# Kernel optimization log

Hardware: AMD Instinct MI355X
Metric: run time of the kernel (lower is better)

## Reference

```python
import jax, jax.numpy as jnp
import numpy as np

EPS = 1e-6     # vnn EPS
BN_EPS = 1e-5  # torch BatchNorm eps


def _vn_batchnorm(x, gamma, beta):
    # x: (B, C, 3, ...). BatchNorm on vector norms (training-mode batch stats).
    norm = jnp.linalg.norm(x, axis=2) + EPS                # (B, C, ...)
    axes = (0,) + tuple(range(2, norm.ndim))
    mean = norm.mean(axis=axes, keepdims=True)
    var = norm.var(axis=axes, keepdims=True)               # biased var, as torch training BN
    shape = (1, -1) + (1,) * (norm.ndim - 2)
    norm_bn = (norm - mean) / jnp.sqrt(var + BN_EPS) * gamma.reshape(shape) + beta.reshape(shape)
    return x / jnp.expand_dims(norm, 2) * jnp.expand_dims(norm_bn, 2)


def _vn_linear_leaky(x, Wf, Wd, gamma, beta):
    # VNLinearLeakyReLU with negative_slope = 0.0
    p = jnp.einsum('oc,bc...->bo...', Wf, x)
    p = _vn_batchnorm(p, gamma, beta)
    d = jnp.einsum('oc,bc...->bo...', Wd, x)
    dot = jnp.sum(p * d, axis=2, keepdims=True)
    dsq = jnp.sum(d * d, axis=2, keepdims=True)
    mask = (dot >= 0).astype(x.dtype)
    return mask * p + (1.0 - mask) * (p - (dot / (dsq + EPS)) * d)


def _graph_feature_cross(x, k):
    # x: (B, 3, N) -> (B, 3, 3, N, k)  channels = [nbr - x, x, x cross nbr]
    xt = jnp.swapaxes(x, 1, 2)                             # (B, N, 3)
    inner = -2.0 * jnp.einsum('bnc,bmc->bnm', xt, xt)      # (B, N, N)
    xx = jnp.sum(x * x, axis=1)                            # (B, N)
    pd = -xx[:, :, None] - inner - xx[:, None, :]          # negative squared distance
    idx = jax.lax.top_k(pd, k)[1]                          # (B, N, k)
    nbr = jax.vmap(lambda pts, i: pts[i])(xt, idx)         # (B, N, k, 3)
    nbr = nbr[:, :, :, None, :]                            # (B, N, k, 1, 3)
    ctr = jnp.broadcast_to(xt[:, :, None, None, :], nbr.shape)
    cross = jnp.cross(nbr, ctr)
    feat = jnp.concatenate([nbr - ctr, ctr, cross], axis=3)  # (B, N, k, 3, 3)
    return jnp.transpose(feat, (0, 3, 4, 1, 2))            # (B, 3, 3, N, k)


def _forward(point_cloud, Wf0, Wd0, g0, b0, Wf1, Wd1, g1, b1, gbn1, bbn1, Wf2, Wd2, g2, b2):
    x = jnp.swapaxes(point_cloud, 1, 2)                    # (B, 3, N)
    num_points = x.shape[1]                                # = 3, faithful to source
    k = min(5, num_points - 1)                             # = 2
    feat = _graph_feature_cross(x, k)                      # (B, 3, 3, N, k)
    out = _vn_linear_leaky(feat, Wf0, Wd0, g0, b0)         # (B, 21, 3, N, k)
    out = out.mean(axis=-1)                                # mean_pool over k -> (B, 21, 3, N)
    out = _vn_linear_leaky(out, Wf1, Wd1, g1, b1)
    out = _vn_batchnorm(out, gbn1, bbn1)
    out = _vn_linear_leaky(out, Wf2, Wd2, g2, b2)          # (B, 4, 3, N)
    # dropout: eval-mode identity
    return out.mean(axis=-1)[:, :3]                        # (B, 3, 3)


def setup_inputs() -> dict:
    key = jax.random.key(0)
    ks = jax.random.split(key, 8)
    B, N = 16, 4096
    C = 21  # 64 // 3
    Co = 4  # 12 // 3
    f32 = jnp.float32
    s3 = 1.0 / np.sqrt(3.0)
    sC = 1.0 / np.sqrt(C)
    return {
        'point_cloud': jax.random.normal(ks[0], (B, N, 3), f32),
        'Wf0': jax.random.normal(ks[1], (C, 3), f32) * s3,
        'Wd0': jax.random.normal(ks[2], (C, 3), f32) * s3,
        'g0': jnp.ones((C,), f32), 'b0': jnp.zeros((C,), f32),
        'Wf1': jax.random.normal(ks[3], (C, C), f32) * sC,
        'Wd1': jax.random.normal(ks[4], (C, C), f32) * sC,
        'g1': jnp.ones((C,), f32), 'b1': jnp.zeros((C,), f32),
        'gbn1': jnp.ones((C,), f32), 'bbn1': jnp.zeros((C,), f32),
        'Wf2': jax.random.normal(ks[5], (Co, C), f32) * sC,
        'Wd2': jax.random.normal(ks[6], (Co, C), f32) * sC,
        'g2': jnp.ones((Co,), f32), 'b2': jnp.zeros((Co,), f32),
    }


def reference(point_cloud, Wf0, Wd0, g0, b0, Wf1, Wd1, g1, b1, gbn1, bbn1, Wf2, Wd2, g2, b2):
    return _forward(point_cloud, Wf0, Wd0, g0, b0, Wf1, Wd1, g1, b1, gbn1, bbn1, Wf2, Wd2, g2, b2)
```

## Files before the change

### kernel.cpp

```cpp
#include <hip/hip_runtime.h>
#include <math.h>

#define B 16
#define N 4096
#define NPTS (B * N)
#define NBK 2048
#define NBT 1024
#define EPSF 1e-6f
#define S8(i) ((i) * 8)

__device__ __forceinline__ float waveReduceSum(float v) {
#pragma unroll
    for (int m = 32; m > 0; m >>= 1) v += __shfl_xor(v, m, 64);
    return v;
}

__device__ __forceinline__ void leaky3(float px, float py, float pz,
                                       float dx, float dy, float dz, float s,
                                       float& ox, float& oy, float& oz) {
    float dotr = px * dx + py * dy + pz * dz;
    float dsq = dx * dx + dy * dy + dz * dz;
    float dot = s * dotr;
    float coef = (dot >= 0.f) ? 0.f : (dot / (dsq + EPSF));
    ox = s * px - coef * dx;
    oy = s * py - coef * dy;
    oz = s * pz - coef * dz;
}

__device__ __forceinline__ void mk_muisd_b(const double* st, int cnt, double M,
                                           float* smu, float* sisd) {
    const int i = threadIdx.x;
    if (i < cnt) {
        double s1 = 0.0, s2 = 0.0;
#pragma unroll
        for (int b = 0; b < B; ++b) {
            s1 += st[S8(b * 2 * cnt + i)];
            s2 += st[S8(b * 2 * cnt + cnt + i)];
        }
        double m = s1 / M;
        double v = s2 / M - m * m;
        smu[i] = (float)m;
        sisd[i] = (float)(1.0 / sqrt(v + 1e-5));
    }
}

struct Feat {
    float cx, cy, cz, e0x, e0y, e0z, e2x, e2y, e2z;
};

__device__ __forceinline__ Feat make_feat(const float* __restrict__ pc,
                                          const int* __restrict__ nbr, int pid) {
    const int b = pid >> 12, n = pid & (N - 1);
    const float* base = pc + (size_t)b * (3 * N);
    Feat f;
    f.cx = base[3 * n];
    f.cy = base[3 * n + 1];
    f.cz = base[3 * n + 2];
    const int jn = nbr[pid];
    float nx = base[3 * jn], ny = base[3 * jn + 1], nz = base[3 * jn + 2];
    f.e0x = nx - f.cx;
    f.e0y = ny - f.cy;
    f.e0z = nz - f.cz;
    f.e2x = ny * f.cz - nz * f.cy;
    f.e2y = nz * f.cx - nx * f.cz;
    f.e2z = nx * f.cy - ny * f.cx;
    return f;
}

#define QW 8
__global__ __launch_bounds__(256) void k_knn(const float* __restrict__ pc,
                                             const float* __restrict__ Wf0,
                                             int* __restrict__ nbrbest,
                                             double* __restrict__ st0) {
    __shared__ float sx[N], sy[N], sz[N];
    __shared__ float ws0[63], sred[168];
    const int b = blockIdx.x >> 7;
    const int qblk = (blockIdx.x & 127) * 32;
    const float* base = pc + (size_t)b * (N * 3);
    for (int j = threadIdx.x; j < N; j += 256) {
        sx[j] = base[3 * j + 0];
        sy[j] = base[3 * j + 1];
        sz[j] = base[3 * j + 2];
    }
    if (threadIdx.x < 63) ws0[threadIdx.x] = Wf0[threadIdx.x];
    __syncthreads();
    const int wid = threadIdx.x >> 6, lane = threadIdx.x & 63;
    const int q0 = qblk + wid * QW;
    float qx[QW], qy[QW], qz[QW], bv[QW];
    int bi[QW], bq[QW];
#pragma unroll
    for (int q = 0; q < QW; ++q) {
        qx[q] = sx[q0 + q];
        qy[q] = sy[q0 + q];
        qz[q] = sz[q0 + q];
        bv[q] = -3.0e38f;
        bi[q] = 0;
    }
#pragma unroll 4
    for (int ch = 0; ch < N / 64; ++ch) {
        const int j = ch * 64 + lane;
        const float xd = sx[j], yd = sy[j], zd = sz[j];
        const float nr2h = -0.5f * (xd * xd + yd * yd + zd * zd);
#pragma unroll
        for (int q = 0; q < QW; ++q) {
            float pd = fmaf(qx[q], xd, fmaf(qy[q], yd, fmaf(qz[q], zd, nr2h)));
            bool upd = (pd > bv[q]) && (j != q0 + q);
            bv[q] = upd ? pd : bv[q];
            bi[q] = upd ? j : bi[q];
        }
    }
#pragma unroll
    for (int q = 0; q < QW; ++q) {
        float a0v = bv[q], a1v = -3.0e38f;
        int a0i = bi[q], a1i = 0x7fffffff;
#pragma unroll
        for (int m = 1; m < 64; m <<= 1) {
            float b0v = __shfl_xor(a0v, m, 64), b1v = __shfl_xor(a1v, m, 64);
            int b0i = __shfl_xor(a0i, m, 64), b1i = __shfl_xor(a1i, m, 64);
            bool bf = (b0v > a0v) || (b0v == a0v && b0i < a0i);
            float c0v = bf ? a0v : b0v;
            int c0i = bf ? a0i : b0i;
            float c1v = bf ? b1v : a1v;
            int c1i = bf ? b1i : a1i;
            a0v = bf ? b0v : a0v;
            a0i = bf ? b0i : a0i;
            bool cf = (c0v > c1v) || (c0v == c1v && c0i < c1i);
            a1v = cf ? c0v : c1v;
            a1i = cf ? c0i : c1i;
        }
        const int i0 = a0i, i1 = a1i;
        double dxa = (double)qx[q] - (double)sx[i0];
        double dya = (double)qy[q] - (double)sy[i0];
        double dza = (double)qz[q] - (double)sz[i0];
        double d0 = dxa * dxa + dya * dya + dza * dza;
        double dxb = (double)qx[q] - (double)sx[i1];
        double dyb = (double)qy[q] - (double)sy[i1];
        double dzb = (double)qz[q] - (double)sz[i1];
        double d1 = dxb * dxb + dyb * dyb + dzb * dzb;
        bool take1 = (d1 < d0) || (d1 == d0 && i1 < i0);
        int best = take1 ? i1 : i0;
        bq[q] = best;
        if (lane == 0) nbrbest[(size_t)b * N + q0 + q] = best;
    }
    if (lane < 21) {
        float s1 = 0.f, s2 = 0.f;
        const float w0 = ws0[3 * lane], w1 = ws0[3 * lane + 1], w2 = ws0[3 * lane + 2];
#pragma unroll
        for (int q = 0; q < QW; ++q) {
            const int sq = q0 + q, jn = bq[q];
            const float cx = sx[sq], cy = sy[sq], cz = sz[sq];
            const float nx = sx[jn], ny = sy[jn], nz = sz[jn];
            const float e0x = nx - cx, e0y = ny - cy, e0z = nz - cz;
            const float e2x = ny * cz - nz * cy;
            const float e2y = nz * cx - nx * cz;
            const float e2z = nx * cy - ny * cx;
            float pSx = w1 * cx, pSy = w1 * cy, pSz = w1 * cz;
            float nS = sqrtf(pSx * pSx + pSy * pSy + pSz * pSz) + EPSF;
            float px = w0 * e0x + w1 * cx + w2 * e2x;
            float py = w0 * e0y + w1 * cy + w2 * e2y;
            float pz = w0 * e0z + w1 * cz + w2 * e2z;
            float nN = sqrtf(px * px + py * py + pz * pz) + EPSF;
            s1 += nS + nN;
            s2 += nS * nS + nN * nN;
        }
        sred[wid * 42 + lane] = s1;
        sred[wid * 42 + 21 + lane] = s2;
    }
    __syncthreads();
    if (threadIdx.x < 42) {
        float p = sred[threadIdx.x] + sred[42 + threadIdx.x] +
                  sred[84 + threadIdx.x] + sred[126 + threadIdx.x];
        atomicAdd(&st0[S8(b * 42 + threadIdx.x)], (double)p);
    }
}

__global__ __launch_bounds__(256) void k_l0st1(
    const float* __restrict__ pc, const int* __restrict__ nbr,
    const float* __restrict__ Wf0, const float* __restrict__ Wd0,
    const float* __restrict__ g0, const float* __restrict__ b0,
    const float* __restrict__ Wf1, const double* __restrict__ st0,
    float* __restrict__ xbuf, double* __restrict__ st1) {
    __shared__ float wf0[63], wd0[63], wf1[441], gg[21], bbs[21], mu[21], isd[21];
    __shared__ float xs[63 * 64];
    if (threadIdx.x < 63) {
        wf0[threadIdx.x] = Wf0[threadIdx.x];
        wd0[threadIdx.x] = Wd0[threadIdx.x];
    }
    for (int i = threadIdx.x; i < 441; i += 256) wf1[i] = Wf1[i];
    if (threadIdx.x < 21) {
        gg[threadIdx.x] = g0[threadIdx.x];
        bbs[threadIdx.x] = b0[threadIdx.x];
    }
    mk_muisd_b(st0, 21, (double)NPTS * 2.0, mu, isd);
    __syncthreads();
    const int lane = threadIdx.x & 63, grp = threadIdx.x >> 6;
    const int pid = blockIdx.x * 64 + lane;
    const int bb = blockIdx.x >> 6;
    Feat f = make_feat(pc, nbr, pid);
    const int cbase = grp * 6;
#pragma unroll
    for (int k = 0; k < 6; ++k) {
        const int c = cbase + k;
        if (c >= 21) break;
        float w0 = wf0[3 * c], w1 = wf0[3 * c + 1], w2 = wf0[3 * c + 2];
        float u0 = wd0[3 * c], u1 = wd0[3 * c + 1], u2 = wd0[3 * c + 2];
        float pSx = w1 * f.cx, pSy = w1 * f.cy, pSz = w1 * f.cz;
        float nS = sqrtf(pSx * pSx + pSy * pSy + pSz * pSz) + EPSF;
        float sS = ((nS - mu[c]) * isd[c] * gg[c] + bbs[c]) / nS;
        float oSx, oSy, oSz;
        leaky3(pSx, pSy, pSz, u1 * f.cx, u1 * f.cy, u1 * f.cz, sS, oSx, oSy, oSz);
        float px = w0 * f.e0x + w1 * f.cx + w2 * f.e2x;
        float py = w0 * f.e0y + w1 * f.cy + w2 * f.e2y;
        float pz = w0 * f.e0z + w1 * f.cz + w2 * f.e2z;
        float dx = u0 * f.e0x + u1 * f.cx + u2 * f.e2x;
        float dy = u0 * f.e0y + u1 * f.cy + u2 * f.e2y;
        float dz = u0 * f.e0z + u1 * f.cz + u2 * f.e2z;
        float nN = sqrtf(px * px + py * py + pz * pz) + EPSF;
        float sN = ((nN - mu[c]) * isd[c] * gg[c] + bbs[c]) / nN;
        float oNx, oNy, oNz;
        leaky3(px, py, pz, dx, dy, dz, sN, oNx, oNy, oNz);
        float x0 = 0.5f * (oSx + oNx), x1 = 0.5f * (oSy + oNy), x2 = 0.5f * (oSz + oNz);
        xs[(3 * c + 0) * 64 + lane] = x0;
        xs[(3 * c + 1) * 64 + lane] = x1;
        xs[(3 * c + 2) * 64 + lane] = x2;
        xbuf[(size_t)(3 * c + 0) * NPTS + pid] = x0;
        xbuf[(size_t)(3 * c + 1) * NPTS + pid] = x1;
        xbuf[(size_t)(3 * c + 2) * NPTS + pid] = x2;
    }
    __syncthreads();
    float xl[63];
#pragma unroll
    for (int ff = 0; ff < 63; ++ff) xl[ff] = xs[ff * 64 + lane];
#pragma unroll
    for (int k = 0; k < 6; ++k) {
        const int c = cbase + k;
        if (c >= 21) break;
        float p0 = 0.f, p1 = 0.f, p2 = 0.f;
#pragma unroll
        for (int j = 0; j < 21; ++j) {
            float w = wf1[c * 21 + j];
            p0 = fmaf(w, xl[3 * j + 0], p0);
            p1 = fmaf(w, xl[3 * j + 1], p1);
            p2 = fmaf(w, xl[3 * j + 2], p2);
        }
        float nn = sqrtf(p0 * p0 + p1 * p1 + p2 * p2) + EPSF;
        float r1 = waveReduceSum(nn);
        float r2 = waveReduceSum(nn * nn);
        if (lane == 0) {
            atomicAdd(&st1[S8(bb * 42 + c)], (double)r1);
            atomicAdd(&st1[S8(bb * 42 + 21 + c)], (double)r2);
        }
    }
}

__global__ __launch_bounds__(256) void k_l1stB(
    float* __restrict__ xbuf, const float* __restrict__ Wf1,
    const float* __restrict__ Wd1, const float* __restrict__ g1,
    const float* __restrict__ b1, const double* __restrict__ st1,
    double* __restrict__ stB) {
    __shared__ float wf1[441], wd1[441], gg[21], bbs[21], mu[21], isd[21];
    for (int i = threadIdx.x; i < 441; i += 256) {
        wf1[i] = Wf1[i];
        wd1[i] = Wd1[i];
    }
    if (threadIdx.x < 21) {
        gg[threadIdx.x] = g1[threadIdx.x];
        bbs[threadIdx.x] = b1[threadIdx.x];
    }
    mk_muisd_b(st1, 21, (double)NPTS, mu, isd);
    __syncthreads();
    const int lane = threadIdx.x & 63, grp = threadIdx.x >> 6;
    const int pid = blockIdx.x * 64 + lane;
    const int bb = blockIdx.x >> 6;
    float xl[63];
#pragma unroll
    for (int ff = 0; ff < 63; ++ff) xl[ff] = xbuf[(size_t)ff * NPTS + pid];
    __syncthreads();
    const int cbase = grp * 6;
#pragma unroll
    for (int k = 0; k < 6; ++k) {
        const int c = cbase + k;
        if (c >= 21) break;
        float p0 = 0.f, p1 = 0.f, p2 = 0.f, d0 = 0.f, d1 = 0.f, d2 = 0.f;
#pragma unroll
        for (int j = 0; j < 21; ++j) {
            float w = wf1[c * 21 + j], u = wd1[c * 21 + j];
            p0 = fmaf(w, xl[3 * j + 0], p0);
            p1 = fmaf(w, xl[3 * j + 1], p1);
            p2 = fmaf(w, xl[3 * j + 2], p2);
            d0 = fmaf(u, xl[3 * j + 0], d0);
            d1 = fmaf(u, xl[3 * j + 1], d1);
            d2 = fmaf(u, xl[3 * j + 2], d2);
        }
        float nn = sqrtf(p0 * p0 + p1 * p1 + p2 * p2) + EPSF;
        float s = ((nn - mu[c]) * isd[c] * gg[c] + bbs[c]) / nn;
        float ox, oy, oz;
        leaky3(p0, p1, p2, d0, d1, d2, s, ox, oy, oz);
        xbuf[(size_t)(3 * c + 0) * NPTS + pid] = ox;
        xbuf[(size_t)(3 * c + 1) * NPTS + pid] = oy;
        xbuf[(size_t)(3 * c + 2) * NPTS + pid] = oz;
        float on = sqrtf(ox * ox + oy * oy + oz * oz) + EPSF;
        float r1 = waveReduceSum(on);
        float r2 = waveReduceSum(on * on);
        if (lane == 0) {
            atomicAdd(&stB[S8(bb * 42 + c)], (double)r1);
            atomicAdd(&stB[S8(bb * 42 + 21 + c)], (double)r2);
        }
    }
}

__global__ __launch_bounds__(256) void k_bn1st2(
    const float* __restrict__ xbuf, const float* __restrict__ gbn,
    const float* __restrict__ bbn, const float* __restrict__ Wf2,
    const double* __restrict__ stB, double* __restrict__ st2) {
    __shared__ float wf2[63], gg[21], bbs[21], mu[21], isd[21];
    __shared__ float zs[63 * 64];
    if (threadIdx.x < 63) wf2[threadIdx.x] = Wf2[threadIdx.x];
    if (threadIdx.x < 21) {
        gg[threadIdx.x] = gbn[threadIdx.x];
        bbs[threadIdx.x] = bbn[threadIdx.x];
    }
    mk_muisd_b(stB, 21, (double)NPTS, mu, isd);
    __syncthreads();
    const int lane = threadIdx.x & 63, grp = threadIdx.x >> 6;
    const int pid = blockIdx.x * 64 + lane;
    const int bb = blockIdx.x >> 6;
    const int cbase = grp * 6;
#pragma unroll
    for (int k = 0; k < 6; ++k) {
        const int c = cbase + k;
        if (c >= 21) break;
        float y0 = xbuf[(size_t)(3 * c + 0) * NPTS + pid];
        float y1 = xbuf[(size_t)(3 * c + 1) * NPTS + pid];
        float y2 = xbuf[(size_t)(3 * c + 2) * NPTS + pid];
        float nn = sqrtf(y0 * y0 + y1 * y1 + y2 * y2) + EPSF;
        float sc = ((nn - mu[c]) * isd[c] * gg[c] + bbs[c]) / nn;
        zs[(3 * c + 0) * 64 + lane] = sc * y0;
        zs[(3 * c + 1) * 64 + lane] = sc * y1;
        zs[(3 * c + 2) * 64 + lane] = sc * y2;
    }
    __syncthreads();
    if (grp < 3) {
        float p0 = 0.f, p1 = 0.f, p2 = 0.f;
#pragma unroll
        for (int j = 0; j < 21; ++j) {
            float w = wf2[grp * 21 + j];
            p0 = fmaf(w, zs[(3 * j + 0) * 64 + lane], p0);
            p1 = fmaf(w, zs[(3 * j + 1) * 64 + lane], p1);
            p2 = fmaf(w, zs[(3 * j + 2) * 64 + lane], p2);
        }
        float nn = sqrtf(p0 * p0 + p1 * p1 + p2 * p2) + EPSF;
        float r1 = waveReduceSum(nn);
        float r2 = waveReduceSum(nn * nn);
        if (lane == 0) {
            atomicAdd(&st2[S8(bb * 6 + grp)], (double)r1);
            atomicAdd(&st2[S8(bb * 6 + 3 + grp)], (double)r2);
        }
    }
}

__global__ __launch_bounds__(256) void k_acc(
    const float* __restrict__ xbuf, const float* __restrict__ gbn,
    const float* __restrict__ bbn, const float* __restrict__ Wf2,
    const float* __restrict__ Wd2, const float* __restrict__ g2,
    const float* __restrict__ b2, const double* __restrict__ stB,
    const double* __restrict__ st2, double* __restrict__ acc) {
    __shared__ float wf2[63], wd2[63], gg[3], bbs[3];
    __shared__ float muB[21], isdB[21], gB[21], bB[21], mu2[3], isd2[3];
    if (threadIdx.x < 63) {
        wf2[threadIdx.x] = Wf2[threadIdx.x];
        wd2[threadIdx.x] = Wd2[threadIdx.x];
    }
    if (threadIdx.x < 21) {
        gB[threadIdx.x] = gbn[threadIdx.x];
        bB[threadIdx.x] = bbn[threadIdx.x];
    }
    if (threadIdx.x < 3) {
        gg[threadIdx.x] = g2[threadIdx.x];
        bbs[threadIdx.x] = b2[threadIdx.x];
    }
    mk_muisd_b(stB, 21, (double)NPTS, muB, isdB);
    mk_muisd_b(st2, 3, (double)NPTS, mu2, isd2);
    __syncthreads();
    const int lane = threadIdx.x & 63, grp = threadIdx.x >> 6;
    if (grp >= 3) return;
    const int pid = blockIdx.x * 64 + lane;
    const int bb = pid >> 12;
    float p0 = 0.f, p1 = 0.f, p2 = 0.f, d0 = 0.f, d1 = 0.f, d2 = 0.f;
#pragma unroll
    for (int j = 0; j < 21; ++j) {
        float y0 = xbuf[(size_t)(3 * j + 0) * NPTS + pid];
        float y1 = xbuf[(size_t)(3 * j + 1) * NPTS + pid];
        float y2 = xbuf[(size_t)(3 * j + 2) * NPTS + pid];
        float nn = sqrtf(y0 * y0 + y1 * y1 + y2 * y2) + EPSF;
        float sc = ((nn - muB[j]) * isdB[j] * gB[j] + bB[j]) / nn;
        float z0 = sc * y0, z1 = sc * y1, z2 = sc * y2;
        float w = wf2[grp * 21 + j], u = wd2[grp * 21 + j];
        p0 = fmaf(w, z0, p0);
        p1 = fmaf(w, z1, p1);
        p2 = fmaf(w, z2, p2);
        d0 = fmaf(u, z0, d0);
        d1 = fmaf(u, z1, d1);
        d2 = fmaf(u, z2, d2);
    }
    float nn = sqrtf(p0 * p0 + p1 * p1 + p2 * p2) + EPSF;
    float s = ((nn - mu2[grp]) * isd2[grp] * gg[grp] + bbs[grp]) / nn;
    float ox, oy, oz;
    leaky3(p0, p1, p2, d0, d1, d2, s, ox, oy, oz);
    float rx = waveReduceSum(ox);
    float ry = waveReduceSum(oy);
    float rz = waveReduceSum(oz);
    if (lane == 0) {
        atomicAdd(&acc[S8(bb * 9 + grp * 3 + 0)], (double)rx);
        atomicAdd(&acc[S8(bb * 9 + grp * 3 + 1)], (double)ry);
        atomicAdd(&acc[S8(bb * 9 + grp * 3 + 2)], (double)rz);
    }
}

__global__ void k_fin(const double* __restrict__ acc, float* __restrict__ out) {
    if (threadIdx.x < B * 9)
        out[threadIdx.x] = (float)(acc[S8(threadIdx.x)] * (1.0 / (double)N));
}

extern "C" void kernel_launch(void* const* d_in, const int* in_sizes, int n_in,
                              void* d_out, int out_size, void* d_ws, size_t ws_size,
                              hipStream_t stream) {
    const float* pc = (const float*)d_in[0];
    const float* Wf0 = (const float*)d_in[1];
    const float* Wd0 = (const float*)d_in[2];
    const float* g0 = (const float*)d_in[3];
    const float* b0 = (const float*)d_in[4];
    const float* Wf1 = (const float*)d_in[5];
    const float* Wd1 = (const float*)d_in[6];
    const float* g1 = (const float*)d_in[7];
    const float* b1 = (const float*)d_in[8];
    const float* gbn1 = (const float*)d_in[9];
    const float* bbn1 = (const float*)d_in[10];
    const float* Wf2 = (const float*)d_in[11];
    const float* Wd2 = (const float*)d_in[12];
    const float* g2 = (const float*)d_in[13];
    const float* b2 = (const float*)d_in[14];
    float* out = (float*)d_out;

    char* ws = (char*)d_ws;
    double* gws = (double*)ws;
    double* st0 = gws;
    double* st1 = gws + S8(672);
    double* stB = gws + S8(1344);
    double* st2 = gws + S8(2016);
    double* acc = gws + S8(2112);
    int* nbrbest = (int*)(ws + 262144);
    float* xbuf = (float*)(ws + 524288);

    hipMemsetAsync(d_ws, 0, 144384, stream);

    k_knn<<<NBK, 256, 0, stream>>>(pc, Wf0, nbrbest, st0);
    k_l0st1<<<NBT, 256, 0, stream>>>(pc, nbrbest, Wf0, Wd0, g0, b0, Wf1, st0,
                                     xbuf, st1);
    k_l1stB<<<NBT, 256, 0, stream>>>(xbuf, Wf1, Wd1, g1, b1, st1, stB);
    k_bn1st2<<<NBT, 256, 0, stream>>>(xbuf, gbn1, bbn1, Wf2, stB, st2);
    k_acc<<<NBT, 256, 0, stream>>>(xbuf, gbn1, bbn1, Wf2, Wd2, g2, b2, stB, st2, acc);
    k_fin<<<1, 256, 0, stream>>>(acc, out);
}
```

Before: 222.7 us.

## Fuse post-kNN layers into one cooperative kernel with grid syncs

Replaces the four per-layer kernels and the final reduction kernel with a single cooperative megakernel. It uses grid.sync at each batch-norm statistics barrier and keeps the per-point 63-float feature tile in shared memory across all stages. This removes the xbuf global round-trips and several kernel launches. In exchange it depends on all 1024 blocks being co-resident, and it falls back to the old kernels if the cooperative launch fails.

```diff
diff --git a/kernel.cpp b/kernel.cpp
--- a/kernel.cpp
+++ b/kernel.cpp
@@ -1,5 +1,8 @@
 #include <hip/hip_runtime.h>
+#include <hip/hip_cooperative_groups.h>
 #include <math.h>
+
+namespace cg = cooperative_groups;
 
 #define B 16
 #define N 4096
@@ -36,6 +39,24 @@
         for (int b = 0; b < B; ++b) {
             s1 += st[S8(b * 2 * cnt + i)];
             s2 += st[S8(b * 2 * cnt + cnt + i)];
+        }
+        double m = s1 / M;
+        double v = s2 / M - m * m;
+        smu[i] = (float)m;
+        sisd[i] = (float)(1.0 / sqrt(v + 1e-5));
+    }
+}
+
+__device__ __forceinline__ void mk_muisd_v(const double* st, int cnt, double M,
+                                           float* smu, float* sisd) {
+    const int i = threadIdx.x;
+    if (i < cnt) {
+        const volatile double* vst = (const volatile double*)st;
+        double s1 = 0.0, s2 = 0.0;
+#pragma unroll
+        for (int b = 0; b < B; ++b) {
+            s1 += vst[S8(b * 2 * cnt + i)];
+            s2 += vst[S8(b * 2 * cnt + cnt + i)];
         }
         double m = s1 / M;
         double v = s2 / M - m * m;
@@ -67,6 +88,30 @@
     return f;
 }
 
+__device__ __forceinline__ void l0_channel(const Feat& f, float w0, float w1,
+                                           float w2, float u0, float u1, float u2,
+                                           float mu, float isd, float g, float bb,
+                                           float& x0, float& x1, float& x2) {
+    float pSx = w1 * f.cx, pSy = w1 * f.cy, pSz = w1 * f.cz;
+    float nS = sqrtf(pSx * pSx + pSy * pSy + pSz * pSz) + EPSF;
+    float sS = ((nS - mu) * isd * g + bb) / nS;
+    float oSx, oSy, oSz;
+    leaky3(pSx, pSy, pSz, u1 * f.cx, u1 * f.cy, u1 * f.cz, sS, oSx, oSy, oSz);
+    float px = w0 * f.e0x + w1 * f.cx + w2 * f.e2x;
+    float py = w0 * f.e0y + w1 * f.cy + w2 * f.e2y;
+    float pz = w0 * f.e0z + w1 * f.cz + w2 * f.e2z;
+    float dx = u0 * f.e0x + u1 * f.cx + u2 * f.e2x;
+    float dy = u0 * f.e0y + u1 * f.cy + u2 * f.e2y;
+    float dz = u0 * f.e0z + u1 * f.cz + u2 * f.e2z;
+    float nN = sqrtf(px * px + py * py + pz * pz) + EPSF;
+    float sN = ((nN - mu) * isd * g + bb) / nN;
+    float oNx, oNy, oNz;
+    leaky3(px, py, pz, dx, dy, dz, sN, oNx, oNy, oNz);
+    x0 = 0.5f * (oSx + oNx);
+    x1 = 0.5f * (oSy + oNy);
+    x2 = 0.5f * (oSz + oNz);
+}
+
 #define QW 8
 __global__ __launch_bounds__(256) void k_knn(const float* __restrict__ pc,
                                              const float* __restrict__ Wf0,
@@ -174,6 +219,230 @@
     }
 }
 
+__global__ __launch_bounds__(256, 4) void k_mega(
+    const float* __restrict__ pc, const int* __restrict__ nbr,
+    const float* __restrict__ Wf0, const float* __restrict__ Wd0,
+    const float* __restrict__ g0, const float* __restrict__ b0,
+    const float* __restrict__ Wf1, const float* __restrict__ Wd1,
+    const float* __restrict__ g1, const float* __restrict__ b1,
+    const float* __restrict__ gbn1, const float* __restrict__ bbn1,
+    const float* __restrict__ Wf2, const float* __restrict__ Wd2,
+    const float* __restrict__ g2, const float* __restrict__ b2,
+    const double* __restrict__ st0, double* __restrict__ st1,
+    double* __restrict__ stB, double* __restrict__ st2,
+    double* __restrict__ acc, float* __restrict__ out) {
+    __shared__ float xs[63 * 64];
+    __shared__ float wf0[63], wd0[63], wf1[441], wd1[441], wf2[63], wd2[63];
+    __shared__ float g0s[21], b0s[21], g1s[21], b1s[21], gBs[21], bBs[21], g2s[3], b2s[3];
+    __shared__ float mu0[21], isd0[21], mu1[21], isd1[21], muB[21], isdB[21], mu2[3], isd2[3];
+    cg::grid_group grid = cg::this_grid();
+    const int lane = threadIdx.x & 63, grp = threadIdx.x >> 6;
+    const int pid = blockIdx.x * 64 + lane;
+    const int bb = blockIdx.x >> 6;
+    const int cbase = grp * 6;
+
+    if (threadIdx.x < 63) {
+        wf0[threadIdx.x] = Wf0[threadIdx.x];
+        wd0[threadIdx.x] = Wd0[threadIdx.x];
+        wf2[threadIdx.x] = Wf2[threadIdx.x];
+        wd2[threadIdx.x] = Wd2[threadIdx.x];
+    }
+    for (int i = threadIdx.x; i < 441; i += 256) {
+        wf1[i] = Wf1[i];
+        wd1[i] = Wd1[i];
+    }
+    if (threadIdx.x < 21) {
+        g0s[threadIdx.x] = g0[threadIdx.x];
+        b0s[threadIdx.x] = b0[threadIdx.x];
+        g1s[threadIdx.x] = g1[threadIdx.x];
+        b1s[threadIdx.x] = b1[threadIdx.x];
+        gBs[threadIdx.x] = gbn1[threadIdx.x];
+        bBs[threadIdx.x] = bbn1[threadIdx.x];
+    }
+    if (threadIdx.x < 3) {
+        g2s[threadIdx.x] = g2[threadIdx.x];
+        b2s[threadIdx.x] = b2[threadIdx.x];
+    }
+    mk_muisd_b(st0, 21, (double)NPTS * 2.0, mu0, isd0);
+    __syncthreads();
+
+    {
+        Feat f = make_feat(pc, nbr, pid);
+#pragma unroll
+        for (int k = 0; k < 6; ++k) {
+            const int c = cbase + k;
+            if (c >= 21) break;
+            float x0, x1, x2;
+            l0_channel(f, wf0[3 * c], wf0[3 * c + 1], wf0[3 * c + 2],
+                       wd0[3 * c], wd0[3 * c + 1], wd0[3 * c + 2],
+                       mu0[c], isd0[c], g0s[c], b0s[c], x0, x1, x2);
+            xs[(3 * c + 0) * 64 + lane] = x0;
+            xs[(3 * c + 1) * 64 + lane] = x1;
+            xs[(3 * c + 2) * 64 + lane] = x2;
+        }
+    }
+    __syncthreads();
+    {
+        float a0[6], a1[6], a2[6];
+#pragma unroll
+        for (int k = 0; k < 6; ++k) { a0[k] = 0.f; a1[k] = 0.f; a2[k] = 0.f; }
+        for (int j = 0; j < 21; ++j) {
+            float x0 = xs[(3 * j + 0) * 64 + lane];
+            float x1 = xs[(3 * j + 1) * 64 + lane];
+            float x2 = xs[(3 * j + 2) * 64 + lane];
+#pragma unroll
+            for (int k = 0; k < 6; ++k) {
+                int cc = cbase + k;
+                cc = cc < 21 ? cc : 20;
+                float w = wf1[cc * 21 + j];
+                a0[k] = fmaf(w, x0, a0[k]);
+                a1[k] = fmaf(w, x1, a1[k]);
+                a2[k] = fmaf(w, x2, a2[k]);
+            }
+        }
+#pragma unroll
+        for (int k = 0; k < 6; ++k) {
+            const int c = cbase + k;
+            if (c >= 21) break;
+            float nn = sqrtf(a0[k] * a0[k] + a1[k] * a1[k] + a2[k] * a2[k]) + EPSF;
+            float r1 = waveReduceSum(nn);
+            float r2 = waveReduceSum(nn * nn);
+            if (lane == 0) {
+                atomicAdd(&st1[S8(bb * 42 + c)], (double)r1);
+                atomicAdd(&st1[S8(bb * 42 + 21 + c)], (double)r2);
+            }
+        }
+    }
+    grid.sync();
+
+    mk_muisd_v(st1, 21, (double)NPTS, mu1, isd1);
+    __syncthreads();
+    {
+        float p0[6], p1[6], p2[6], q0[6], q1[6], q2[6];
+#pragma unroll
+        for (int k = 0; k < 6; ++k) {
+            p0[k] = 0.f; p1[k] = 0.f; p2[k] = 0.f;
+            q0[k] = 0.f; q1[k] = 0.f; q2[k] = 0.f;
+        }
+        for (int j = 0; j < 21; ++j) {
+            float x0 = xs[(3 * j + 0) * 64 + lane];
+            float x1 = xs[(3 * j + 1) * 64 + lane];
+            float x2 = xs[(3 * j + 2) * 64 + lane];
+#pragma unroll
+            for (int k = 0; k < 6; ++k) {
+                int cc = cbase + k;
+                cc = cc < 21 ? cc : 20;
+                float w = wf1[cc * 21 + j], u = wd1[cc * 21 + j];
+                p0[k] = fmaf(w, x0, p0[k]);
+                p1[k] = fmaf(w, x1, p1[k]);
+                p2[k] = fmaf(w, x2, p2[k]);
+                q0[k] = fmaf(u, x0, q0[k]);
+                q1[k] = fmaf(u, x1, q1[k]);
+                q2[k] = fmaf(u, x2, q2[k]);
+            }
+        }
+        float sn1[6], sn2[6];
+#pragma unroll
+        for (int k = 0; k < 6; ++k) {
+            int cc = cbase + k;
+            cc = cc < 21 ? cc : 20;
+            float nn = sqrtf(p0[k] * p0[k] + p1[k] * p1[k] + p2[k] * p2[k]) + EPSF;
+            float s = ((nn - mu1[cc]) * isd1[cc] * g1s[cc] + b1s[cc]) / nn;
+            float ox, oy, oz;
+            leaky3(p0[k], p1[k], p2[k], q0[k], q1[k], q2[k], s, ox, oy, oz);
+            p0[k] = ox; p1[k] = oy; p2[k] = oz;
+            float on = sqrtf(ox * ox + oy * oy + oz * oz) + EPSF;
+            sn1[k] = on;
+            sn2[k] = on * on;
+        }
+        __syncthreads();
+#pragma unroll
+        for (int k = 0; k < 6; ++k) {
+            const int c = cbase + k;
+            if (c >= 21) break;
+            xs[(3 * c + 0) * 64 + lane] = p0[k];
+            xs[(3 * c + 1) * 64 + lane] = p1[k];
+            xs[(3 * c + 2) * 64 + lane] = p2[k];
+            float r1 = waveReduceSum(sn1[k]);
+            float r2 = waveReduceSum(sn2[k]);
+            if (lane == 0) {
+                atomicAdd(&stB[S8(bb * 42 + c)], (double)r1);
+                atomicAdd(&stB[S8(bb * 42 + 21 + c)], (double)r2);
+            }
+        }
+    }
+    grid.sync();
+
+    mk_muisd_v(stB, 21, (double)NPTS, muB, isdB);
+    __syncthreads();
+#pragma unroll
+    for (int k = 0; k < 6; ++k) {
+        const int c = cbase + k;
+        if (c >= 21) break;
+        float y0 = xs[(3 * c + 0) * 64 + lane];
+        float y1 = xs[(3 * c + 1) * 64 + lane];
+        float y2 = xs[(3 * c + 2) * 64 + lane];
+        float nn = sqrtf(y0 * y0 + y1 * y1 + y2 * y2) + EPSF;
+        float sc = ((nn - muB[c]) * isdB[c] * gBs[c] + bBs[c]) / nn;
+        xs[(3 * c + 0) * 64 + lane] = sc * y0;
+        xs[(3 * c + 1) * 64 + lane] = sc * y1;
+        xs[(3 * c + 2) * 64 + lane] = sc * y2;
+    }
+    __syncthreads();
+    if (grp < 3) {
+        float p0 = 0.f, p1 = 0.f, p2 = 0.f;
+        for (int j = 0; j < 21; ++j) {
+            float w = wf2[grp * 21 + j];
+            p0 = fmaf(w, xs[(3 * j + 0) * 64 + lane], p0);
+            p1 = fmaf(w, xs[(3 * j + 1) * 64 + lane], p1);
+            p2 = fmaf(w, xs[(3 * j + 2) * 64 + lane], p2);
+        }
+        float nn = sqrtf(p0 * p0 + p1 * p1 + p2 * p2) + EPSF;
+        float r1 = waveReduceSum(nn);
+        float r2 = waveReduceSum(nn * nn);
+        if (lane == 0) {
+            atomicAdd(&st2[S8(bb * 6 + grp)], (double)r1);
+            atomicAdd(&st2[S8(bb * 6 + 3 + grp)], (double)r2);
+        }
+    }
+    grid.sync();
+
+    mk_muisd_v(st2, 3, (double)NPTS, mu2, isd2);
+    __syncthreads();
+    if (grp < 3) {
+        float p0 = 0.f, p1 = 0.f, p2 = 0.f, d0 = 0.f, d1 = 0.f, d2 = 0.f;
+        for (int j = 0; j < 21; ++j) {
+            float z0 = xs[(3 * j + 0) * 64 + lane];
+            float z1 = xs[(3 * j + 1) * 64 + lane];
+            float z2 = xs[(3 * j + 2) * 64 + lane];
+            float w = wf2[grp * 21 + j], u = wd2[grp * 21 + j];
+            p0 = fmaf(w, z0, p0);
+            p1 = fmaf(w, z1, p1);
+            p2 = fmaf(w, z2, p2);
+            d0 = fmaf(u, z0, d0);
+            d1 = fmaf(u, z1, d1);
+            d2 = fmaf(u, z2, d2);
+        }
+        float nn = sqrtf(p0 * p0 + p1 * p1 + p2 * p2) + EPSF;
+        float s = ((nn - mu2[grp]) * isd2[grp] * g2s[grp] + b2s[grp]) / nn;
+        float ox, oy, oz;
+        leaky3(p0, p1, p2, d0, d1, d2, s, ox, oy, oz);
+        float rx = waveReduceSum(ox);
+        float ry = waveReduceSum(oy);
+        float rz = waveReduceSum(oz);
+        if (lane == 0) {
+            atomicAdd(&acc[S8(bb * 9 + grp * 3 + 0)], (double)rx);
+            atomicAdd(&acc[S8(bb * 9 + grp * 3 + 1)], (double)ry);
+            atomicAdd(&acc[S8(bb * 9 + grp * 3 + 2)], (double)rz);
+        }
+    }
+    grid.sync();
+    if (blockIdx.x == 0 && threadIdx.x < B * 9) {
+        const volatile double* va = (const volatile double*)acc;
+        out[threadIdx.x] = (float)(va[S8(threadIdx.x)] * (1.0 / (double)N));
+    }
+}
+
 __global__ __launch_bounds__(256) void k_l0st1(
     const float* __restrict__ pc, const int* __restrict__ nbr,
     const float* __restrict__ Wf0, const float* __restrict__ Wd0,
@@ -202,24 +471,10 @@
     for (int k = 0; k < 6; ++k) {
         const int c = cbase + k;
         if (c >= 21) break;
-        float w0 = wf0[3 * c], w1 = wf0[3 * c + 1], w2 = wf0[3 * c + 2];
-        float u0 = wd0[3 * c], u1 = wd0[3 * c + 1], u2 = wd0[3 * c + 2];
-        float pSx = w1 * f.cx, pSy = w1 * f.cy, pSz = w1 * f.cz;
-        float nS = sqrtf(pSx * pSx + pSy * pSy + pSz * pSz) + EPSF;
-        float sS = ((nS - mu[c]) * isd[c] * gg[c] + bbs[c]) / nS;
-        float oSx, oSy, oSz;
-        leaky3(pSx, pSy, pSz, u1 * f.cx, u1 * f.cy, u1 * f.cz, sS, oSx, oSy, oSz);
-        float px = w0 * f.e0x + w1 * f.cx + w2 * f.e2x;
-        float py = w0 * f.e0y + w1 * f.cy + w2 * f.e2y;
-        float pz = w0 * f.e0z + w1 * f.cz + w2 * f.e2z;
-        float dx = u0 * f.e0x + u1 * f.cx + u2 * f.e2x;
-        float dy = u0 * f.e0y + u1 * f.cy + u2 * f.e2y;
-        float dz = u0 * f.e0z + u1 * f.cz + u2 * f.e2z;
-        float nN = sqrtf(px * px + py * py + pz * pz) + EPSF;
-        float sN = ((nN - mu[c]) * isd[c] * gg[c] + bbs[c]) / nN;
-        float oNx, oNy, oNz;
-        leaky3(px, py, pz, dx, dy, dz, sN, oNx, oNy, oNz);
-        float x0 = 0.5f * (oSx + oNx), x1 = 0.5f * (oSy + oNy), x2 = 0.5f * (oSz + oNz);
+        float x0, x1, x2;
+        l0_channel(f, wf0[3 * c], wf0[3 * c + 1], wf0[3 * c + 2],
+                   wd0[3 * c], wd0[3 * c + 1], wd0[3 * c + 2],
+                   mu[c], isd[c], gg[c], bbs[c], x0, x1, x2);
         xs[(3 * c + 0) * 64 + lane] = x0;
         xs[(3 * c + 1) * 64 + lane] = x1;
         xs[(3 * c + 2) * 64 + lane] = x2;
@@ -455,10 +710,25 @@
     hipMemsetAsync(d_ws, 0, 144384, stream);
 
     k_knn<<<NBK, 256, 0, stream>>>(pc, Wf0, nbrbest, st0);
-    k_l0st1<<<NBT, 256, 0, stream>>>(pc, nbrbest, Wf0, Wd0, g0, b0, Wf1, st0,
-                                     xbuf, st1);
-    k_l1stB<<<NBT, 256, 0, stream>>>(xbuf, Wf1, Wd1, g1, b1, st1, stB);
-    k_bn1st2<<<NBT, 256, 0, stream>>>(xbuf, gbn1, bbn1, Wf2, stB, st2);
-    k_acc<<<NBT, 256, 0, stream>>>(xbuf, gbn1, bbn1, Wf2, Wd2, g2, b2, stB, st2, acc);
-    k_fin<<<1, 256, 0, stream>>>(acc, out);
-}
+
+    const int* nbrc = nbrbest;
+    const double* st0c = st0;
+    void* args[] = {(void*)&pc, (void*)&nbrc,
+                    (void*)&Wf0, (void*)&Wd0, (void*)&g0, (void*)&b0,
+                    (void*)&Wf1, (void*)&Wd1, (void*)&g1, (void*)&b1,
+                    (void*)&gbn1, (void*)&bbn1,
+                    (void*)&Wf2, (void*)&Wd2, (void*)&g2, (void*)&b2,
+                    (void*)&st0c, (void*)&st1, (void*)&stB, (void*)&st2,
+                    (void*)&acc, (void*)&out};
+    hipError_t e = hipLaunchCooperativeKernel((void*)k_mega, dim3(NBT), dim3(256),
+                                              args, 0, stream);
+    if (e != hipSuccess) {
+        k_l0st1<<<NBT, 256, 0, stream>>>(pc, nbrbest, Wf0, Wd0, g0, b0, Wf1, st0,
+                                         xbuf, st1);
+        k_l1stB<<<NBT, 256, 0, stream>>>(xbuf, Wf1, Wd1, g1, b1, st1, stB);
+        k_bn1st2<<<NBT, 256, 0, stream>>>(xbuf, gbn1, bbn1, Wf2, stB, st2);
+        k_acc<<<NBT, 256, 0, stream>>>(xbuf, gbn1, bbn1, Wf2, Wd2, g2, b2, stB,
+                                       st2, acc);
+        k_fin<<<1, 256, 0, stream>>>(acc, out);
+    }
+}
```

Result: slower. 727.9 us (+226.8%).
